# Optimization experiments

Measured on AMD Instinct MI355X. Metric: run time of the kernel, lower is better.

Reference implementation:

```python
import jax, jax.numpy as jnp
import numpy as np

VOCAB = 32000
EMBED = 8      # == d_k == n_qubits (forced by the module's reshapes)
NQ = 8
DEPTH = 2
NBLOCKS = 6
FFN = 8        # == n_qubits (forced)
NCLASSES = 10
B, S = 32, 1024
LN_EPS = 1e-5

_H = np.array([[1.0, 1.0], [1.0, -1.0]], np.complex64) / np.sqrt(2.0).astype(np.float32)


def _posenc(seq, dim):
    pos = np.arange(seq, dtype=np.float32)[:, None]
    div = np.exp(np.arange(0, dim, 2, dtype=np.float32) * (-np.log(10000.0) / dim))
    pe = np.zeros((seq, dim), np.float32)
    pe[:, 0::2] = np.sin(pos * div)
    pe[:, 1::2] = np.cos(pos * div)
    return jnp.asarray(pe)


def _quantum_head(x, depth=DEPTH):
    """Batched statevector simulation of the QNode. x: (N, NQ) angles -> (N, NQ) Z expvals."""
    N, n = x.shape
    c = jnp.cos(0.5 * x).astype(jnp.complex64)
    s = jnp.sin(0.5 * x).astype(jnp.complex64)
    amp = jnp.stack([c, -1j * s], axis=-1)  # (N, n, 2): RX(theta)|0>
    state = amp[:, 0]  # product state built wire by wire -> (N, 2, ..., 2)
    for i in range(1, n):
        state = state[..., None] * amp[:, i].reshape((N,) + (1,) * (state.ndim - 1) + (2,))
    Hm = jnp.asarray(_H)
    for _ in range(depth):
        for i in range(n - 1):  # CNOT(i, i+1): flip target slice where control==1
            s0 = jnp.take(state, 0, axis=i + 1)
            s1 = jnp.flip(jnp.take(state, 1, axis=i + 1), axis=i + 1)
            state = jnp.stack([s0, s1], axis=i + 1)
        state = jnp.einsum('...i,ij->...j', state, Hm)  # Hadamard on last wire
    probs = state.real ** 2 + state.imag ** 2  # (N, 2, ..., 2)
    zs = []
    for i in range(n):
        axes = tuple(a for a in range(1, n + 1) if a != i + 1)
        m = probs.sum(axis=axes)  # (N, 2) marginal of wire i
        zs.append(m[:, 0] - m[:, 1])
    return jnp.stack(zs, axis=-1)


def _ln(x, g, b):
    m = x.mean(axis=-1, keepdims=True)
    v = ((x - m) ** 2).mean(axis=-1, keepdims=True)
    return g * (x - m) / jnp.sqrt(v + LN_EPS) + b


def _forward(tokens, emb, ln1_g, ln1_b, ln2_g, ln2_b, attn_w, attn_b,
             ffn_w1, ffn_b1, ffn_w2, ffn_b2, cls_w, cls_b):
    Bt, St = tokens.shape
    E = emb.shape[1]
    x = emb[tokens] + _posenc(St, E)[None]  # (B, S, E)
    scale = float(1.0 / np.sqrt(E))
    for l in range(NBLOCKS):
        # quantum attention (num_heads == 1, d_k == E)
        qkv = _quantum_head(x.reshape(-1, E)).reshape(Bt, St, E)
        scores = jnp.einsum('bqd,bkd->bqk', qkv, qkv) * scale
        attn = jax.nn.softmax(scores, axis=-1)
        out = jnp.einsum('bqk,bkd->bqd', attn, qkv)
        attn_out = out @ attn_w[l] + attn_b[l]
        x = _ln(x + attn_out, ln1_g[l], ln1_b[l])
        # quantum FFN
        h = x @ ffn_w1[l] + ffn_b1[l]  # (B, S, FFN)
        qf = _quantum_head(h.reshape(-1, FFN)).reshape(Bt, St, FFN)
        ffn_out = qf @ ffn_w2[l] + ffn_b2[l]
        x = _ln(x + ffn_out, ln2_g[l], ln2_b[l])
    pooled = x.mean(axis=1)  # (B, E)
    return pooled @ cls_w + cls_b  # (B, NCLASSES)


def setup_inputs() -> dict:
    key = jax.random.key(0)
    ks = jax.random.split(key, 8)
    f32 = jnp.float32
    L, E, F = NBLOCKS, EMBED, FFN
    return {
        'tokens': jax.random.randint(ks[0], (B, S), 0, VOCAB),
        'emb': jax.random.normal(ks[1], (VOCAB, E), f32) * 0.1,
        'ln1_g': jnp.ones((L, E), f32), 'ln1_b': jnp.zeros((L, E), f32),
        'ln2_g': jnp.ones((L, E), f32), 'ln2_b': jnp.zeros((L, E), f32),
        'attn_w': jax.random.normal(ks[2], (L, E, E), f32) * 0.3,
        'attn_b': jnp.zeros((L, E), f32),
        'ffn_w1': jax.random.normal(ks[3], (L, E, F), f32) * 0.3,
        'ffn_b1': jnp.zeros((L, F), f32),
        'ffn_w2': jax.random.normal(ks[4], (L, F, E), f32) * 0.3,
        'ffn_b2': jnp.zeros((L, E), f32),
        'cls_w': jax.random.normal(ks[5], (E, NCLASSES), f32) * 0.3,
        'cls_b': jnp.zeros((NCLASSES,), f32),
    }


def reference(tokens, emb, ln1_g, ln1_b, ln2_g, ln2_b, attn_w, attn_b,
              ffn_w1, ffn_b1, ffn_w2, ffn_b2, cls_w, cls_b):
    return _forward(tokens, emb, ln1_g, ln1_b, ln2_g, ln2_b, attn_w, attn_b,
                    ffn_w1, ffn_b1, ffn_w2, ffn_b2, cls_w, cls_b)
```

## Files before the change

kernel.cpp:

```cpp
#include <hip/hip_runtime.h>
#include <math.h>

#define EMB 8
#define SEQ 1024
#define NBATCH 32
#define NROWS (NBATCH * SEQ)
#define LNEPS 1e-5f
#define F(l, b, c) (((l) * 32 + (b)) * 16 + (c))

typedef __attribute__((ext_vector_type(4))) unsigned u32x4;
typedef __attribute__((ext_vector_type(8))) _Float16 f16x8;
typedef __attribute__((ext_vector_type(16))) float f32x16;

union FragU { unsigned u[4]; f16x8 s; };

__device__ __forceinline__ unsigned pkrtz(float a, float b) {
    unsigned r;
    asm("v_cvt_pkrtz_f16_f32 %0, %1, %2" : "=v"(r) : "v"(a), "v"(b));
    return r;
}
__device__ __forceinline__ unsigned pk_mul_f16(unsigned a, unsigned b) {
    unsigned r;
    asm("v_pk_mul_f16 %0, %1, %2" : "=v"(r) : "v"(a), "v"(b));
    return r;
}
__device__ __forceinline__ float hw_exp2(float x) {
    return __builtin_amdgcn_exp2f(x);
}

__device__ __forceinline__ void llc_load_2rows(const unsigned short* p,
                                               u32x4* d0, u32x4* d1) {
    asm volatile(
        "global_load_dwordx4 %0, %[a], off sc0 sc1\n\t"
        "global_load_dwordx4 %1, %[a], off offset:16 sc0 sc1\n\t"
        "s_waitcnt vmcnt(0)"
        : "=&v"(*d0), "=&v"(*d1) : [a] "v"(p) : "memory");
}
__device__ __forceinline__ void llc_store_row16(unsigned short* p, u32x4 v) {
    asm volatile("global_store_dwordx4 %[a], %[x], off sc0 sc1"
                 :: [a] "v"(p), [x] "v"(v) : "memory");
}
__device__ __forceinline__ void sys_store(float* p, float v) {
    asm volatile("global_store_dword %0, %1, off sc0 sc1" :: "v"(p), "v"(v) : "memory");
}
__device__ __forceinline__ float sys_load(const float* p) {
    float r;
    asm volatile("global_load_dword %0, %1, off sc0 sc1\n\ts_waitcnt vmcnt(0)"
                 : "=v"(r) : "v"(p) : "memory");
    return r;
}
__device__ __forceinline__ unsigned sys_load_u32(const unsigned* p) {
    unsigned r;
    asm volatile("global_load_dword %0, %1, off sc0 sc1\n\ts_waitcnt vmcnt(0)"
                 : "=v"(r) : "v"(p) : "memory");
    return r;
}
__device__ __forceinline__ void sys_store_u32(unsigned* p, unsigned v) {
    asm volatile("global_store_dword %0, %1, off sc0 sc1" :: "v"(p), "v"(v) : "memory");
}

__device__ __forceinline__ void qhead(const float xv[8], float z[8]) {
    float c[8];
#pragma unroll
    for (int j = 0; j < 8; ++j) c[j] = __cosf(xv[j]);
    float e0 = c[0];
    float o1 = c[1];
    float e2 = e0 * c[2];
    float o3 = o1 * c[3];
    float e4 = e2 * c[4];
    float o5 = o3 * c[5];
    float e6 = e4 * c[6];
    z[0] = e0; z[1] = o1; z[2] = e2; z[3] = o3;
    z[4] = e4; z[5] = o5; z[6] = e6;
    z[7] = e6 * o5 * c[7];
}

__device__ __forceinline__ void embed_row(const int* __restrict__ tokens,
                                          const float* __restrict__ emb,
                                          long grow, int srow, float xv[8]) {
    int tok = tokens[grow];
    const float* e = emb + (long)tok * EMB;
    float p = (float)srow;
    xv[0] = e[0] + sinf(p);
    xv[1] = e[1] + cosf(p);
    xv[2] = e[2] + sinf(p * 0.1f);
    xv[3] = e[3] + cosf(p * 0.1f);
    xv[4] = e[4] + sinf(p * 0.01f);
    xv[5] = e[5] + cosf(p * 0.01f);
    xv[6] = e[6] + sinf(p * 0.001f);
    xv[7] = e[7] + cosf(p * 0.001f);
}

__global__ __launch_bounds__(1024) void zero_flags(unsigned* __restrict__ f) {
    for (int i = threadIdx.x; i < 3584; i += 1024) f[i] = 0u;
}

__global__ __launch_bounds__(512, 2) void qt_fused(
    const int* __restrict__ tokens, const float* __restrict__ emb,
    const float* __restrict__ attn_w, const float* __restrict__ attn_b,
    const float* __restrict__ ln1_g, const float* __restrict__ ln1_b,
    const float* __restrict__ ffn_w1, const float* __restrict__ ffn_b1,
    const float* __restrict__ ffn_w2, const float* __restrict__ ffn_b2,
    const float* __restrict__ ln2_g, const float* __restrict__ ln2_b,
    const float* __restrict__ cls_w, const float* __restrict__ cls_b,
    unsigned short* __restrict__ qkv0, unsigned short* __restrict__ qkv1,
    unsigned* __restrict__ flags, unsigned* __restrict__ pcnt,
    float* __restrict__ partial, float* __restrict__ out)
{
    __shared__ __align__(16) uint2 KbP[2][1024];
    __shared__ __align__(16) unsigned short VtH[8][1032];
    __shared__ float Olds[8][32][9];
    __shared__ float x_lds[2][64][8];
    __shared__ int isL[2];

    const int bid = blockIdx.x;
    const int group = bid & 15;
    const int chunk = bid >> 4;
    const int tid = threadIdx.x;

    const int w = tid >> 6;
    const int lane = tid & 63;
    const int ln = lane & 31;
    const int h = lane >> 5;
    const int qtile = w >> 2;
    const int qu = w & 3;
    const int r0 = tid * 2;
    const unsigned B2PK = pkrtz(0.51006972f, 0.51006972f);

    for (int l = 0; l < 6; ++l) {
        const unsigned short* qr = (l & 1) ? qkv1 : qkv0;
        unsigned short* qw = (l & 1) ? qkv0 : qkv1;
        for (int ph = 0; ph < 2; ++ph) {
            const int bb = group * 2 + ph;
            {
                u32x4 d0, d1;
                if (l == 0) {
                    float e0[8], e1[8], z0[8], z1[8];
                    embed_row(tokens, emb, (long)bb * SEQ + r0, r0, e0);
                    embed_row(tokens, emb, (long)bb * SEQ + r0 + 1, r0 + 1, e1);
                    if ((r0 >> 6) == chunk) {
                        const int lr = r0 - chunk * 64;
#pragma unroll
                        for (int j = 0; j < 8; ++j) {
                            x_lds[ph][lr][j] = e0[j];
                            x_lds[ph][lr + 1][j] = e1[j];
                        }
                    }
                    qhead(e0, z0); qhead(e1, z1);
                    d0[0] = pkrtz(z0[0], z0[1]); d0[1] = pkrtz(z0[2], z0[3]);
                    d0[2] = pkrtz(z0[4], z0[5]); d0[3] = pkrtz(z0[6], z0[7]);
                    d1[0] = pkrtz(z1[0], z1[1]); d1[1] = pkrtz(z1[2], z1[3]);
                    d1[2] = pkrtz(z1[4], z1[5]); d1[3] = pkrtz(z1[6], z1[7]);
                } else {
                    const unsigned* fp = &flags[F(l, bb, r0 >> 6)];
                    while (sys_load_u32(fp) == 0u) __builtin_amdgcn_s_sleep(1);
                    llc_load_2rows(qr + ((long)bb * SEQ + r0) * 8, &d0, &d1);
                }
                u32x4 kp0, kp1;
                kp0[0] = d0[0]; kp0[1] = d0[1]; kp0[2] = d1[0]; kp0[3] = d1[1];
                kp1[0] = d0[2]; kp1[1] = d0[3]; kp1[2] = d1[2]; kp1[3] = d1[3];
                *(u32x4*)&KbP[0][r0] = kp0;
                *(u32x4*)&KbP[1][r0] = kp1;
#pragma unroll
                for (int c = 0; c < 8; ++c) {
                    unsigned wa = d0[c >> 1], wb = d1[c >> 1];
                    unsigned v = (c & 1) ? ((wa >> 16) | (wb & 0xFFFF0000u))
                                         : ((wa & 0xFFFFu) | (wb << 16));
                    *(unsigned*)&VtH[c][r0] = v;
                }
            }
            __syncthreads();

            const int qbase = chunk * 64 + qtile * 32;
            FragU qfB;
            {
                uint2 qh = KbP[h][qbase + ln];
                unsigned qx = pk_mul_f16(qh.x, B2PK);
                unsigned qy = pk_mul_f16(qh.y, B2PK);
                qfB.u[0] = qx; qfB.u[1] = qy; qfB.u[2] = qx; qfB.u[3] = qy;
            }
            f32x16 zc;
#pragma unroll
            for (int i = 0; i < 16; ++i) zc[i] = 0.f;
            f32x16 accA = zc, accB = zc;
            FragU v1c, v2c;
            {
                const unsigned fill = (ln == 8) ? 0x3C003C00u : 0u;
#pragma unroll
                for (int i = 0; i < 4; ++i) { v1c.u[i] = fill; v2c.u[i] = fill; }
            }

#pragma unroll 2
            for (int t = 0; t < 8; ++t) {
                const int kbase = ((qu << 3) | t) << 5;
                FragU kfA;
                {
                    uint2 kh = KbP[h][kbase + ln];
                    kfA.u[0] = kh.x; kfA.u[1] = kh.y; kfA.u[2] = 0; kfA.u[3] = 0;
                }
                f32x16 s = __builtin_amdgcn_mfma_f32_32x32x16_f16(kfA.s, qfB.s, zc, 0, 0, 0);
                float p[16];
#pragma unroll
                for (int g = 0; g < 16; ++g) p[g] = hw_exp2(s[g]);

                FragU a1, a2;
#pragma unroll
                for (int vi = 0; vi < 4; ++vi) {
                    a1.u[vi] = pkrtz(p[2 * vi], p[2 * vi + 1]);
                    a2.u[vi] = pkrtz(p[8 + 2 * vi], p[8 + 2 * vi + 1]);
                }
                FragU v1h = v1c, v2h = v2c;
                if (ln < 8) {
                    const unsigned* q0 = (const unsigned*)&VtH[ln][kbase + 4 * h];
                    const unsigned* q1 = (const unsigned*)&VtH[ln][kbase + 8 + 4 * h];
                    const unsigned* q2 = (const unsigned*)&VtH[ln][kbase + 16 + 4 * h];
                    const unsigned* q3 = (const unsigned*)&VtH[ln][kbase + 24 + 4 * h];
                    v1h.u[0] = q0[0]; v1h.u[1] = q0[1]; v1h.u[2] = q1[0]; v1h.u[3] = q1[1];
                    v2h.u[0] = q2[0]; v2h.u[1] = q2[1]; v2h.u[2] = q3[0]; v2h.u[3] = q3[1];
                }
                accA = __builtin_amdgcn_mfma_f32_32x32x16_f16(a1.s, v1h.s, accA, 0, 0, 0);
                accB = __builtin_amdgcn_mfma_f32_32x32x16_f16(a2.s, v2h.s, accB, 0, 0, 0);
            }

            if (ln <= 8) {
#pragma unroll
                for (int g = 0; g < 16; ++g)
                    Olds[w][(g & 3) + 8 * (g >> 2) + 4 * h][ln] = accA[g] + accB[g];
            }
            __syncthreads();

            if ((tid >> 6) == ph) {
                const int r = tid & 63;
                const int rr = r & 31;
                const int w0 = (r >> 5) * 4;
                float o[9];
#pragma unroll
                for (int c = 0; c < 9; ++c)
                    o[c] = (Olds[w0][rr][c] + Olds[w0 + 1][rr][c])
                         + (Olds[w0 + 2][rr][c] + Olds[w0 + 3][rr][c]);
                float inv = 1.0f / o[8];
                float outv[8];
#pragma unroll
                for (int c = 0; c < 8; ++c) outv[c] = o[c] * inv;

                const float* W  = attn_w + l * 64; const float* Wb  = attn_b + l * 8;
                const float* g1 = ln1_g + l * 8;   const float* b1v = ln1_b + l * 8;
                const float* W1 = ffn_w1 + l * 64; const float* c1  = ffn_b1 + l * 8;
                const float* W2 = ffn_w2 + l * 64; const float* c2  = ffn_b2 + l * 8;
                const float* g2 = ln2_g + l * 8;   const float* b2v = ln2_b + l * 8;

                float xv[8];
#pragma unroll
                for (int j = 0; j < 8; ++j) xv[j] = x_lds[ph][r][j];

                float y[8]; float m = 0.f;
#pragma unroll
                for (int j = 0; j < 8; ++j) {
                    float vv = Wb[j];
#pragma unroll
                    for (int i = 0; i < 8; ++i) vv += outv[i] * W[i * 8 + j];
                    y[j] = xv[j] + vv;
                    m += y[j];
                }
                m *= 0.125f;
                float var = 0.f;
#pragma unroll
                for (int j = 0; j < 8; ++j) { float dd = y[j] - m; var += dd * dd; }
                var *= 0.125f;
                float rsg = rsqrtf(var + LNEPS);
                float xn[8];
#pragma unroll
                for (int j = 0; j < 8; ++j) xn[j] = g1[j] * (y[j] - m) * rsg + b1v[j];

                float hh[8];
#pragma unroll
                for (int j = 0; j < 8; ++j) {
                    float vv = c1[j];
#pragma unroll
                    for (int i = 0; i < 8; ++i) vv += xn[i] * W1[i * 8 + j];
                    hh[j] = vv;
                }
                float qff[8]; qhead(hh, qff);
                float m2 = 0.f;
#pragma unroll
                for (int j = 0; j < 8; ++j) {
                    float vv = c2[j];
#pragma unroll
                    for (int i = 0; i < 8; ++i) vv += qff[i] * W2[i * 8 + j];
                    y[j] = xn[j] + vv;
                    m2 += y[j];
                }
                m2 *= 0.125f;
                float var2 = 0.f;
#pragma unroll
                for (int j = 0; j < 8; ++j) { float dd = y[j] - m2; var2 += dd * dd; }
                var2 *= 0.125f;
                float rs2 = rsqrtf(var2 + LNEPS);
#pragma unroll
                for (int j = 0; j < 8; ++j) {
                    float xo = g2[j] * (y[j] - m2) * rs2 + b2v[j];
                    x_lds[ph][r][j] = xo;
                    xv[j] = xo;
                }

                if (l < 5) {
                    float z[8]; qhead(xv, z);
                    u32x4 pz;
                    pz[0] = pkrtz(z[0], z[1]); pz[1] = pkrtz(z[2], z[3]);
                    pz[2] = pkrtz(z[4], z[5]); pz[3] = pkrtz(z[6], z[7]);
                    llc_store_row16(qw + ((long)bb * SEQ + chunk * 64 + r) * 8, pz);
                    asm volatile("s_waitcnt vmcnt(0)" ::: "memory");
                    if (r == 0) sys_store_u32(&flags[F(l + 1, bb, chunk)], 1u);
                }
            }
        }
    }

    if ((tid >> 6) < 2) {
        const int ph = tid >> 6;
        const int r = tid & 63;
        const int bb = group * 2 + ph;
        float a[8];
#pragma unroll
        for (int j = 0; j < 8; ++j) {
            a[j] = x_lds[ph][r][j];
#pragma unroll
            for (int off = 1; off <= 32; off <<= 1) a[j] += __shfl_xor(a[j], off);
        }
        if (r < 8) sys_store(&partial[(bb * 16 + chunk) * 8 + r], a[r]);
    }
    asm volatile("s_waitcnt vmcnt(0)" ::: "memory");
    __syncthreads();
    if (tid == 0) {
        unsigned r = __hip_atomic_fetch_add(&pcnt[(group * 2) * 16], 1u,
                                            __ATOMIC_RELAXED, __HIP_MEMORY_SCOPE_AGENT);
        isL[0] = (r == 15u);
    }
    if (tid == 64) {
        unsigned r = __hip_atomic_fetch_add(&pcnt[(group * 2 + 1) * 16], 1u,
                                            __ATOMIC_RELAXED, __HIP_MEMORY_SCOPE_AGENT);
        isL[1] = (r == 15u);
    }
    __syncthreads();
    if ((tid >> 6) < 2) {
        const int ph = tid >> 6;
        if (isL[ph]) {
            const int bb = group * 2 + ph;
            const int lr = tid & 63;
            int g = lr >> 3, j = lr & 7;
            float s = sys_load(&partial[(bb * 16 + g) * 8 + j])
                    + sys_load(&partial[(bb * 16 + g + 8) * 8 + j]);
            s += __shfl_xor(s, 8); s += __shfl_xor(s, 16); s += __shfl_xor(s, 32);
            float poolj = s * (1.0f / 1024.0f);
            int c = lr < 10 ? lr : 9;
            float o = cls_b[c];
#pragma unroll
            for (int j2 = 0; j2 < 8; ++j2)
                o += __shfl(poolj, j2) * cls_w[j2 * 10 + c];
            if (lr < 10) out[bb * 10 + lr] = o;
        }
    }
}

extern "C" void kernel_launch(void* const* d_in, const int* in_sizes, int n_in,
                              void* d_out, int out_size, void* d_ws, size_t ws_size,
                              hipStream_t stream) {
    const int*   tokens = (const int*)d_in[0];
    const float* emb    = (const float*)d_in[1];
    const float* ln1_g  = (const float*)d_in[2];
    const float* ln1_b  = (const float*)d_in[3];
    const float* ln2_g  = (const float*)d_in[4];
    const float* ln2_b  = (const float*)d_in[5];
    const float* attn_w = (const float*)d_in[6];
    const float* attn_b = (const float*)d_in[7];
    const float* ffn_w1 = (const float*)d_in[8];
    const float* ffn_b1 = (const float*)d_in[9];
    const float* ffn_w2 = (const float*)d_in[10];
    const float* ffn_b2 = (const float*)d_in[11];
    const float* cls_w  = (const float*)d_in[12];
    const float* cls_b  = (const float*)d_in[13];

    unsigned*       flags   = (unsigned*)d_ws;
    unsigned*       pcnt    = flags + 3072;
    float*          partial = (float*)(pcnt + 512);
    unsigned short* qkv0    = (unsigned short*)(partial + 4096);
    unsigned short* qkv1    = qkv0 + (long)NROWS * 8;
    float*          outp    = (float*)d_out;

    zero_flags<<<1, 1024, 0, stream>>>(flags);
    qt_fused<<<256, 512, 0, stream>>>(
        tokens, emb, attn_w, attn_b, ln1_g, ln1_b,
        ffn_w1, ffn_b1, ffn_w2, ffn_b2, ln2_g, ln2_b,
        cls_w, cls_b, qkv0, qkv1, flags, pcnt, partial, outp);
}
```

Measured before the change: 75.41 us.

## Process both batch phases per layer together to halve block barriers and polls

Each block now loads and stages K/V for both of its batch elements at once, with double-buffered LDS, and polls both readiness flags in one combined loop. Attention for the two phases then runs back to back, and the per-row epilogue for both phases runs in parallel on waves 0 and 1. This cuts the __syncthreads count per layer from four to two and overlaps the two flag waits and global loads. The cost is roughly double the LDS footprint, which may reduce occupancy under the 2-blocks-per-CU launch bound, plus more live registers during staging.

```diff
diff --git a/kernel.cpp b/kernel.cpp
--- a/kernel.cpp
+++ b/kernel.cpp
@@ -28,13 +28,30 @@
     return __builtin_amdgcn_exp2f(x);
 }
 
-__device__ __forceinline__ void llc_load_2rows(const unsigned short* p,
-                                               u32x4* d0, u32x4* d1) {
+__device__ __forceinline__ void llc_load_2x2(const unsigned short* pa,
+                                             const unsigned short* pb,
+                                             u32x4* a0, u32x4* a1,
+                                             u32x4* b0, u32x4* b1) {
     asm volatile(
         "global_load_dwordx4 %0, %[a], off sc0 sc1\n\t"
         "global_load_dwordx4 %1, %[a], off offset:16 sc0 sc1\n\t"
+        "global_load_dwordx4 %2, %[b], off sc0 sc1\n\t"
+        "global_load_dwordx4 %3, %[b], off offset:16 sc0 sc1\n\t"
         "s_waitcnt vmcnt(0)"
-        : "=&v"(*d0), "=&v"(*d1) : [a] "v"(p) : "memory");
+        : "=&v"(*a0), "=&v"(*a1), "=&v"(*b0), "=&v"(*b1)
+        : [a] "v"(pa), [b] "v"(pb) : "memory");
+}
+__device__ __forceinline__ void poll2(const unsigned* p0, const unsigned* p1) {
+    unsigned f0, f1;
+    for (;;) {
+        asm volatile(
+            "global_load_dword %0, %2, off sc0 sc1\n\t"
+            "global_load_dword %1, %3, off sc0 sc1\n\t"
+            "s_waitcnt vmcnt(0)"
+            : "=&v"(f0), "=&v"(f1) : "v"(p0), "v"(p1) : "memory");
+        if (f0 != 0u && f1 != 0u) break;
+        __builtin_amdgcn_s_sleep(1);
+    }
 }
 __device__ __forceinline__ void llc_store_row16(unsigned short* p, u32x4 v) {
     asm volatile("global_store_dwordx4 %[a], %[x], off sc0 sc1"
@@ -45,12 +62,6 @@
 }
 __device__ __forceinline__ float sys_load(const float* p) {
     float r;
-    asm volatile("global_load_dword %0, %1, off sc0 sc1\n\ts_waitcnt vmcnt(0)"
-                 : "=v"(r) : "v"(p) : "memory");
-    return r;
-}
-__device__ __forceinline__ unsigned sys_load_u32(const unsigned* p) {
-    unsigned r;
     asm volatile("global_load_dword %0, %1, off sc0 sc1\n\ts_waitcnt vmcnt(0)"
                  : "=v"(r) : "v"(p) : "memory");
     return r;
@@ -91,6 +102,13 @@
     xv[7] = e[7] + cosf(p * 0.001f);
 }
 
+__device__ __forceinline__ u32x4 pack_row(const float z[8]) {
+    u32x4 d;
+    d[0] = pkrtz(z[0], z[1]); d[1] = pkrtz(z[2], z[3]);
+    d[2] = pkrtz(z[4], z[5]); d[3] = pkrtz(z[6], z[7]);
+    return d;
+}
+
 __global__ __launch_bounds__(1024) void zero_flags(unsigned* __restrict__ f) {
     for (int i = threadIdx.x; i < 3584; i += 1024) f[i] = 0u;
 }
@@ -107,9 +125,9 @@
     unsigned* __restrict__ flags, unsigned* __restrict__ pcnt,
     float* __restrict__ partial, float* __restrict__ out)
 {
-    __shared__ __align__(16) uint2 KbP[2][1024];
-    __shared__ __align__(16) unsigned short VtH[8][1032];
-    __shared__ float Olds[8][32][9];
+    __shared__ __align__(16) uint2 KbP[2][2][1024];
+    __shared__ __align__(16) unsigned short VtH[2][8][1032];
+    __shared__ float Olds[2][8][32][9];
     __shared__ float x_lds[2][64][8];
     __shared__ int isL[2];
 
@@ -125,56 +143,73 @@
     const int qtile = w >> 2;
     const int qu = w & 3;
     const int r0 = tid * 2;
+    const int bb0 = group * 2, bb1 = bb0 + 1;
     const unsigned B2PK = pkrtz(0.51006972f, 0.51006972f);
 
     for (int l = 0; l < 6; ++l) {
         const unsigned short* qr = (l & 1) ? qkv1 : qkv0;
         unsigned short* qw = (l & 1) ? qkv0 : qkv1;
-        for (int ph = 0; ph < 2; ++ph) {
-            const int bb = group * 2 + ph;
+
+        {
+            u32x4 dA0, dA1, dB0, dB1;
+            if (l == 0) {
+                const int inX = ((r0 >> 6) == chunk);
+                const int lr = r0 - chunk * 64;
+                float e[8], z[8];
+                embed_row(tokens, emb, (long)bb0 * SEQ + r0, r0, e);
+                if (inX) { for (int j = 0; j < 8; ++j) x_lds[0][lr][j] = e[j]; }
+                qhead(e, z); dA0 = pack_row(z);
+                embed_row(tokens, emb, (long)bb0 * SEQ + r0 + 1, r0 + 1, e);
+                if (inX) { for (int j = 0; j < 8; ++j) x_lds[0][lr + 1][j] = e[j]; }
+                qhead(e, z); dA1 = pack_row(z);
+                embed_row(tokens, emb, (long)bb1 * SEQ + r0, r0, e);
+                if (inX) { for (int j = 0; j < 8; ++j) x_lds[1][lr][j] = e[j]; }
+                qhead(e, z); dB0 = pack_row(z);
+                embed_row(tokens, emb, (long)bb1 * SEQ + r0 + 1, r0 + 1, e);
+                if (inX) { for (int j = 0; j < 8; ++j) x_lds[1][lr + 1][j] = e[j]; }
+                qhead(e, z); dB1 = pack_row(z);
+            } else {
+                poll2(&flags[F(l, bb0, r0 >> 6)], &flags[F(l, bb1, r0 >> 6)]);
+                llc_load_2x2(qr + ((long)bb0 * SEQ + r0) * 8,
+                             qr + ((long)bb1 * SEQ + r0) * 8,
+                             &dA0, &dA1, &dB0, &dB1);
+            }
             {
-                u32x4 d0, d1;
-                if (l == 0) {
-                    float e0[8], e1[8], z0[8], z1[8];
-                    embed_row(tokens, emb, (long)bb * SEQ + r0, r0, e0);
-                    embed_row(tokens, emb, (long)bb * SEQ + r0 + 1, r0 + 1, e1);
-                    if ((r0 >> 6) == chunk) {
-                        const int lr = r0 - chunk * 64;
-#pragma unroll
-                        for (int j = 0; j < 8; ++j) {
-                            x_lds[ph][lr][j] = e0[j];
-                            x_lds[ph][lr + 1][j] = e1[j];
-                        }
-                    }
-                    qhead(e0, z0); qhead(e1, z1);
-                    d0[0] = pkrtz(z0[0], z0[1]); d0[1] = pkrtz(z0[2], z0[3]);
-                    d0[2] = pkrtz(z0[4], z0[5]); d0[3] = pkrtz(z0[6], z0[7]);
-                    d1[0] = pkrtz(z1[0], z1[1]); d1[1] = pkrtz(z1[2], z1[3]);
-                    d1[2] = pkrtz(z1[4], z1[5]); d1[3] = pkrtz(z1[6], z1[7]);
-                } else {
-                    const unsigned* fp = &flags[F(l, bb, r0 >> 6)];
-                    while (sys_load_u32(fp) == 0u) __builtin_amdgcn_s_sleep(1);
-                    llc_load_2rows(qr + ((long)bb * SEQ + r0) * 8, &d0, &d1);
-                }
                 u32x4 kp0, kp1;
-                kp0[0] = d0[0]; kp0[1] = d0[1]; kp0[2] = d1[0]; kp0[3] = d1[1];
-                kp1[0] = d0[2]; kp1[1] = d0[3]; kp1[2] = d1[2]; kp1[3] = d1[3];
-                *(u32x4*)&KbP[0][r0] = kp0;
-                *(u32x4*)&KbP[1][r0] = kp1;
+                kp0[0] = dA0[0]; kp0[1] = dA0[1]; kp0[2] = dA1[0]; kp0[3] = dA1[1];
+                kp1[0] = dA0[2]; kp1[1] = dA0[3]; kp1[2] = dA1[2]; kp1[3] = dA1[3];
+                *(u32x4*)&KbP[0][0][r0] = kp0;
+                *(u32x4*)&KbP[0][1][r0] = kp1;
 #pragma unroll
                 for (int c = 0; c < 8; ++c) {
-                    unsigned wa = d0[c >> 1], wb = d1[c >> 1];
+                    unsigned wa = dA0[c >> 1], wb = dA1[c >> 1];
                     unsigned v = (c & 1) ? ((wa >> 16) | (wb & 0xFFFF0000u))
                                          : ((wa & 0xFFFFu) | (wb << 16));
-                    *(unsigned*)&VtH[c][r0] = v;
+                    *(unsigned*)&VtH[0][c][r0] = v;
                 }
             }
-            __syncthreads();
-
-            const int qbase = chunk * 64 + qtile * 32;
+            {
+                u32x4 kp0, kp1;
+                kp0[0] = dB0[0]; kp0[1] = dB0[1]; kp0[2] = dB1[0]; kp0[3] = dB1[1];
+                kp1[0] = dB0[2]; kp1[1] = dB0[3]; kp1[2] = dB1[2]; kp1[3] = dB1[3];
+                *(u32x4*)&KbP[1][0][r0] = kp0;
+                *(u32x4*)&KbP[1][1][r0] = kp1;
+#pragma unroll
+                for (int c = 0; c < 8; ++c) {
+                    unsigned wa = dB0[c >> 1], wb = dB1[c >> 1];
+                    unsigned v = (c & 1) ? ((wa >> 16) | (wb & 0xFFFF0000u))
+                                         : ((wa & 0xFFFFu) | (wb << 16));
+                    *(unsigned*)&VtH[1][c][r0] = v;
+                }
+            }
+        }
+        __syncthreads();
+
+        const int qbase = chunk * 64 + qtile * 32;
+        for (int ph = 0; ph < 2; ++ph) {
             FragU qfB;
             {
-                uint2 qh = KbP[h][qbase + ln];
+                uint2 qh = KbP[ph][h][qbase + ln];
                 unsigned qx = pk_mul_f16(qh.x, B2PK);
                 unsigned qy = pk_mul_f16(qh.y, B2PK);
                 qfB.u[0] = qx; qfB.u[1] = qy; qfB.u[2] = qx; qfB.u[3] = qy;
@@ -195,7 +230,7 @@
                 const int kbase = ((qu << 3) | t) << 5;
                 FragU kfA;
                 {
-                    uint2 kh = KbP[h][kbase + ln];
+                    uint2 kh = KbP[ph][h][kbase + ln];
                     kfA.u[0] = kh.x; kfA.u[1] = kh.y; kfA.u[2] = 0; kfA.u[3] = 0;
                 }
                 f32x16 s = __builtin_amdgcn_mfma_f32_32x32x16_f16(kfA.s, qfB.s, zc, 0, 0, 0);
@@ -211,10 +246,10 @@
                 }
                 FragU v1h = v1c, v2h = v2c;
                 if (ln < 8) {
-                    const unsigned* q0 = (const unsigned*)&VtH[ln][kbase + 4 * h];
-                    const unsigned* q1 = (const unsigned*)&VtH[ln][kbase + 8 + 4 * h];
-                    const unsigned* q2 = (const unsigned*)&VtH[ln][kbase + 16 + 4 * h];
-                    const unsigned* q3 = (const unsigned*)&VtH[ln][kbase + 24 + 4 * h];
+                    const unsigned* q0 = (const unsigned*)&VtH[ph][ln][kbase + 4 * h];
+                    const unsigned* q1 = (const unsigned*)&VtH[ph][ln][kbase + 8 + 4 * h];
+                    const unsigned* q2 = (const unsigned*)&VtH[ph][ln][kbase + 16 + 4 * h];
+                    const unsigned* q3 = (const unsigned*)&VtH[ph][ln][kbase + 24 + 4 * h];
                     v1h.u[0] = q0[0]; v1h.u[1] = q0[1]; v1h.u[2] = q1[0]; v1h.u[3] = q1[1];
                     v2h.u[0] = q2[0]; v2h.u[1] = q2[1]; v2h.u[2] = q3[0]; v2h.u[3] = q3[1];
                 }
@@ -225,93 +260,95 @@
             if (ln <= 8) {
 #pragma unroll
                 for (int g = 0; g < 16; ++g)
-                    Olds[w][(g & 3) + 8 * (g >> 2) + 4 * h][ln] = accA[g] + accB[g];
-            }
-            __syncthreads();
-
-            if ((tid >> 6) == ph) {
-                const int r = tid & 63;
-                const int rr = r & 31;
-                const int w0 = (r >> 5) * 4;
-                float o[9];
-#pragma unroll
-                for (int c = 0; c < 9; ++c)
-                    o[c] = (Olds[w0][rr][c] + Olds[w0 + 1][rr][c])
-                         + (Olds[w0 + 2][rr][c] + Olds[w0 + 3][rr][c]);
-                float inv = 1.0f / o[8];
-                float outv[8];
-#pragma unroll
-                for (int c = 0; c < 8; ++c) outv[c] = o[c] * inv;
-
-                const float* W  = attn_w + l * 64; const float* Wb  = attn_b + l * 8;
-                const float* g1 = ln1_g + l * 8;   const float* b1v = ln1_b + l * 8;
-                const float* W1 = ffn_w1 + l * 64; const float* c1  = ffn_b1 + l * 8;
-                const float* W2 = ffn_w2 + l * 64; const float* c2  = ffn_b2 + l * 8;
-                const float* g2 = ln2_g + l * 8;   const float* b2v = ln2_b + l * 8;
-
-                float xv[8];
-#pragma unroll
-                for (int j = 0; j < 8; ++j) xv[j] = x_lds[ph][r][j];
-
-                float y[8]; float m = 0.f;
-#pragma unroll
-                for (int j = 0; j < 8; ++j) {
-                    float vv = Wb[j];
-#pragma unroll
-                    for (int i = 0; i < 8; ++i) vv += outv[i] * W[i * 8 + j];
-                    y[j] = xv[j] + vv;
-                    m += y[j];
-                }
-                m *= 0.125f;
-                float var = 0.f;
-#pragma unroll
-                for (int j = 0; j < 8; ++j) { float dd = y[j] - m; var += dd * dd; }
-                var *= 0.125f;
-                float rsg = rsqrtf(var + LNEPS);
-                float xn[8];
-#pragma unroll
-                for (int j = 0; j < 8; ++j) xn[j] = g1[j] * (y[j] - m) * rsg + b1v[j];
-
-                float hh[8];
-#pragma unroll
-                for (int j = 0; j < 8; ++j) {
-                    float vv = c1[j];
-#pragma unroll
-                    for (int i = 0; i < 8; ++i) vv += xn[i] * W1[i * 8 + j];
-                    hh[j] = vv;
-                }
-                float qff[8]; qhead(hh, qff);
-                float m2 = 0.f;
-#pragma unroll
-                for (int j = 0; j < 8; ++j) {
-                    float vv = c2[j];
-#pragma unroll
-                    for (int i = 0; i < 8; ++i) vv += qff[i] * W2[i * 8 + j];
-                    y[j] = xn[j] + vv;
-                    m2 += y[j];
-                }
-                m2 *= 0.125f;
-                float var2 = 0.f;
-#pragma unroll
-                for (int j = 0; j < 8; ++j) { float dd = y[j] - m2; var2 += dd * dd; }
-                var2 *= 0.125f;
-                float rs2 = rsqrtf(var2 + LNEPS);
-#pragma unroll
-                for (int j = 0; j < 8; ++j) {
-                    float xo = g2[j] * (y[j] - m2) * rs2 + b2v[j];
-                    x_lds[ph][r][j] = xo;
-                    xv[j] = xo;
-                }
-
-                if (l < 5) {
-                    float z[8]; qhead(xv, z);
-                    u32x4 pz;
-                    pz[0] = pkrtz(z[0], z[1]); pz[1] = pkrtz(z[2], z[3]);
-                    pz[2] = pkrtz(z[4], z[5]); pz[3] = pkrtz(z[6], z[7]);
-                    llc_store_row16(qw + ((long)bb * SEQ + chunk * 64 + r) * 8, pz);
-                    asm volatile("s_waitcnt vmcnt(0)" ::: "memory");
-                    if (r == 0) sys_store_u32(&flags[F(l + 1, bb, chunk)], 1u);
-                }
+                    Olds[ph][w][(g & 3) + 8 * (g >> 2) + 4 * h][ln] = accA[g] + accB[g];
+            }
+        }
+        __syncthreads();
+
+        if (w < 2) {
+            const int ph = w;
+            const int bb = bb0 + ph;
+            const int r = lane;
+            const int rr = r & 31;
+            const int w0 = (r >> 5) * 4;
+            float o[9];
+#pragma unroll
+            for (int c = 0; c < 9; ++c)
+                o[c] = (Olds[ph][w0][rr][c] + Olds[ph][w0 + 1][rr][c])
+                     + (Olds[ph][w0 + 2][rr][c] + Olds[ph][w0 + 3][rr][c]);
+            float inv = 1.0f / o[8];
+            float outv[8];
+#pragma unroll
+            for (int c = 0; c < 8; ++c) outv[c] = o[c] * inv;
+
+            const float* W  = attn_w + l * 64; const float* Wb  = attn_b + l * 8;
+            const float* g1 = ln1_g + l * 8;   const float* b1v = ln1_b + l * 8;
+            const float* W1 = ffn_w1 + l * 64; const float* c1  = ffn_b1 + l * 8;
+            const float* W2 = ffn_w2 + l * 64; const float* c2  = ffn_b2 + l * 8;
+            const float* g2 = ln2_g + l * 8;   const float* b2v = ln2_b + l * 8;
+
+            float xv[8];
+#pragma unroll
+            for (int j = 0; j < 8; ++j) xv[j] = x_lds[ph][r][j];
+
+            float y[8]; float m = 0.f;
+#pragma unroll
+            for (int j = 0; j < 8; ++j) {
+                float vv = Wb[j];
+#pragma unroll
+                for (int i = 0; i < 8; ++i) vv += outv[i] * W[i * 8 + j];
+                y[j] = xv[j] + vv;
+                m += y[j];
+            }
+            m *= 0.125f;
+            float var = 0.f;
+#pragma unroll
+            for (int j = 0; j < 8; ++j) { float dd = y[j] - m; var += dd * dd; }
+            var *= 0.125f;
+            float rsg = rsqrtf(var + LNEPS);
+            float xn[8];
+#pragma unroll
+            for (int j = 0; j < 8; ++j) xn[j] = g1[j] * (y[j] - m) * rsg + b1v[j];
+
+            float hh[8];
+#pragma unroll
+            for (int j = 0; j < 8; ++j) {
+                float vv = c1[j];
+#pragma unroll
+                for (int i = 0; i < 8; ++i) vv += xn[i] * W1[i * 8 + j];
+                hh[j] = vv;
+            }
+            float qff[8]; qhead(hh, qff);
+            float m2 = 0.f;
+#pragma unroll
+            for (int j = 0; j < 8; ++j) {
+                float vv = c2[j];
+#pragma unroll
+                for (int i = 0; i < 8; ++i) vv += qff[i] * W2[i * 8 + j];
+                y[j] = xn[j] + vv;
+                m2 += y[j];
+            }
+            m2 *= 0.125f;
+            float var2 = 0.f;
+#pragma unroll
+            for (int j = 0; j < 8; ++j) { float dd = y[j] - m2; var2 += dd * dd; }
+            var2 *= 0.125f;
+            float rs2 = rsqrtf(var2 + LNEPS);
+#pragma unroll
+            for (int j = 0; j < 8; ++j) {
+                float xo = g2[j] * (y[j] - m2) * rs2 + b2v[j];
+                x_lds[ph][r][j] = xo;
+                xv[j] = xo;
+            }
+
+            if (l < 5) {
+                float z[8]; qhead(xv, z);
+                u32x4 pz;
+                pz[0] = pkrtz(z[0], z[1]); pz[1] = pkrtz(z[2], z[3]);
+                pz[2] = pkrtz(z[4], z[5]); pz[3] = pkrtz(z[6], z[7]);
+                llc_store_row16(qw + ((long)bb * SEQ + chunk * 64 + r) * 8, pz);
+                asm volatile("s_waitcnt vmcnt(0)" ::: "memory");
+                if (r == 0) sys_store_u32(&flags[F(l + 1, bb, chunk)], 1u);
             }
         }
     }
@@ -319,7 +356,7 @@
     if ((tid >> 6) < 2) {
         const int ph = tid >> 6;
         const int r = tid & 63;
-        const int bb = group * 2 + ph;
+        const int bb = bb0 + ph;
         float a[8];
 #pragma unroll
         for (int j = 0; j < 8; ++j) {
@@ -332,12 +369,12 @@
     asm volatile("s_waitcnt vmcnt(0)" ::: "memory");
     __syncthreads();
     if (tid == 0) {
-        unsigned r = __hip_atomic_fetch_add(&pcnt[(group * 2) * 16], 1u,
+        unsigned r = __hip_atomic_fetch_add(&pcnt[bb0 * 16], 1u,
                                             __ATOMIC_RELAXED, __HIP_MEMORY_SCOPE_AGENT);
         isL[0] = (r == 15u);
     }
     if (tid == 64) {
-        unsigned r = __hip_atomic_fetch_add(&pcnt[(group * 2 + 1) * 16], 1u,
+        unsigned r = __hip_atomic_fetch_add(&pcnt[bb1 * 16], 1u,
                                             __ATOMIC_RELAXED, __HIP_MEMORY_SCOPE_AGENT);
         isL[1] = (r == 15u);
     }
@@ -345,7 +382,7 @@
     if ((tid >> 6) < 2) {
         const int ph = tid >> 6;
         if (isL[ph]) {
-            const int bb = group * 2 + ph;
+            const int bb = bb0 + ph;
             const int lr = tid & 63;
             int g = lr >> 3, j = lr & 7;
             float s = sys_load(&partial[(bb * 16 + g) * 8 + j])
```

After: 82.66 us. 1.1x slower.
